# Optimization experiments

Hardware: AMD Instinct MI355X
Metric: run time of the kernel (lower is better)

## Reference

```python
import jax, jax.numpy as jnp
import numpy as np

N = 100000      # atoms
E = 1200000     # edges
N0 = 3125       # crystals
ORIG = 92
NBR = 41
AF = 64
NCONV = 3
HF = 128
EPS = 1e-5


def _bn(x, g, b):
    # training-mode BatchNorm1d: biased batch stats over axis 0
    m = jnp.mean(x, axis=0)
    v = jnp.var(x, axis=0)
    return (x - m) * jax.lax.rsqrt(v + EPS) * g + b


def setup_inputs() -> dict:
    key = jax.random.key(0)
    ks = jax.random.split(key, 16)
    inp = {}
    inp["atom_fea"] = jax.random.normal(ks[0], (N, ORIG), dtype=jnp.float32)
    inp["nbr_fea"] = jax.random.normal(ks[1], (E, NBR), dtype=jnp.float32)
    inp["self_fea_idx"] = jnp.sort(jax.random.randint(ks[2], (E,), 0, N))
    inp["nbr_fea_idx"] = jax.random.randint(ks[3], (E,), 0, N)
    inp["crystal_atom_idx"] = jnp.sort(jax.random.randint(ks[4], (N,), 0, N0))
    s = 0.05
    inp["emb_W"] = jax.random.normal(ks[5], (ORIG, AF), dtype=jnp.float32) * s
    inp["emb_b"] = jnp.zeros((AF,), dtype=jnp.float32)
    inp["conv_W"] = jax.random.normal(ks[6], (NCONV, 2 * AF + NBR, 2 * AF), dtype=jnp.float32) * s
    inp["conv_b"] = jnp.zeros((NCONV, 2 * AF), dtype=jnp.float32)
    inp["bn1_g"] = jnp.ones((NCONV, 2 * AF), dtype=jnp.float32)
    inp["bn1_b"] = jnp.zeros((NCONV, 2 * AF), dtype=jnp.float32)
    inp["bn2_g"] = jnp.ones((NCONV, AF), dtype=jnp.float32)
    inp["bn2_b"] = jnp.zeros((NCONV, AF), dtype=jnp.float32)
    inp["fc1_W"] = jax.random.normal(ks[7], (AF, HF), dtype=jnp.float32) * s
    inp["fc1_b"] = jnp.zeros((HF,), dtype=jnp.float32)
    inp["out_W"] = jax.random.normal(ks[8], (HF, 1), dtype=jnp.float32) * s
    inp["out_b"] = jnp.zeros((1,), dtype=jnp.float32)
    return inp


def reference(atom_fea, nbr_fea, self_fea_idx, nbr_fea_idx, crystal_atom_idx,
              emb_W, emb_b, conv_W, conv_b, bn1_g, bn1_b, bn2_g, bn2_b,
              fc1_W, fc1_b, out_W, out_b):
    sp = jax.nn.softplus
    x = atom_fea @ emb_W + emb_b                       # (N, AF)
    for i in range(NCONV):
        total = jnp.concatenate(
            [x[self_fea_idx], x[nbr_fea_idx], nbr_fea], axis=1)  # (E, 2*AF+NBR)
        total = total @ conv_W[i] + conv_b[i]                    # (E, 2*AF)
        total = _bn(total, bn1_g[i], bn1_b[i])
        filt, core = jnp.split(total, 2, axis=1)
        msg = jax.nn.sigmoid(filt) * sp(core)                    # (E, AF)
        summed = jax.ops.segment_sum(msg, self_fea_idx, num_segments=N)
        x = sp(x + _bn(summed, bn2_g[i], bn2_b[i]))
    # mean pooling over atoms per crystal
    crys_sum = jax.ops.segment_sum(x, crystal_atom_idx, num_segments=N0)
    counts = jax.ops.segment_sum(jnp.ones((N,), dtype=x.dtype),
                                 crystal_atom_idx, num_segments=N0)
    crys = crys_sum / jnp.maximum(counts, 1.0)[:, None]          # (N0, AF)
    crys = sp(sp(crys) @ fc1_W + fc1_b)                          # (N0, HF)
    return crys @ out_W + out_b                                  # (N0, 1)
```

## Files before the change

kernel.cpp:

```cpp
#include <hip/hip_runtime.h>
#include <hip/hip_bf16.h>
#include <hip/hip_fp16.h>

#define N_ATOM 100000
#define N_EDGE 1200000
#define N_CRYS 3125
#define EPSF 1e-5f

typedef __attribute__((ext_vector_type(8))) short bf16x8;
typedef __attribute__((ext_vector_type(4))) float f32x4;

__device__ __forceinline__ float fexp(float x) {
    return __builtin_amdgcn_exp2f(x * 1.4426950408889634f);
}
__device__ __forceinline__ float flog(float x) {
    return __builtin_amdgcn_logf(x) * 0.6931471805599453f;
}
__device__ __forceinline__ float frcp(float x) { return __builtin_amdgcn_rcpf(x); }

__device__ __forceinline__ float softplusf(float x) {
    return fmaxf(x, 0.f) + flog(1.f + fexp(-fabsf(x)));
}
__device__ __forceinline__ float sigmoidf(float x) {
    return frcp(1.f + fexp(-x));
}

__device__ __forceinline__ float ldf(const void* p, long i, int isf32) {
    return isf32 ? ((const float*)p)[i]
                 : __bfloat162float(((const __hip_bfloat16*)p)[i]);
}

__global__ void detect_dtype(const unsigned short* __restrict__ af,
                             int* __restrict__ flag) {
    __shared__ int cnt;
    if (threadIdx.x == 0) cnt = 0;
    __syncthreads();
    int c = 0;
    for (int i = threadIdx.x; i < 4096; i += 256) {
        int e = (af[i] >> 7) & 0xFF;
        if (e >= 100 && e <= 140) c++;
    }
    atomicAdd(&cnt, c);
    __syncthreads();
    if (threadIdx.x == 0) flag[0] = (cnt < 3300) ? 1 : 0;
}

__global__ void cvt_params(const void* embW, const void* embb, const void* bn1g,
                           const void* bn1b, const void* bn2g, const void* bn2b,
                           const void* fc1W, const void* fc1b, const void* outW,
                           const void* outb, const int* __restrict__ flag,
                           float* __restrict__ dst) {
    int f = flag[0];
    const void* ps[10] = {embW, embb, bn1g, bn1b, bn2g, bn2b, fc1W, fc1b, outW, outb};
    const int off[10]  = {0, 5888, 5952, 6336, 6720, 6912, 7104, 15296, 15424, 15552};
    const int n[10]    = {5888, 64, 384, 384, 192, 192, 8192, 128, 128, 1};
    for (int it = 0; it < 10; ++it)
        for (int i = threadIdx.x; i < n[it]; i += 256)
            dst[off[it] + i] = ldf(ps[it], i, f);
}


__global__ void pad_nbr(const void* __restrict__ nf, const int* __restrict__ flag,
                        __hip_bfloat16* __restrict__ np_) {
    int f = flag[0];
    long i = (long)blockIdx.x * 256 + threadIdx.x;
    long e = i >> 6;
    int  k = (int)(i & 63);
    float v = (k < 41) ? ldf(nf, e * 41 + k, f) : 0.f;
    np_[i] = __float2bfloat16(v);
}

__global__ void pack_W(const void* __restrict__ convW, const int* __restrict__ flag,
                       __hip_bfloat16* __restrict__ wf) {
    int f = flag[0];
    int b = blockIdx.x;
    int l = threadIdx.x;
    int t = b & 7;
    int c = (b >> 3) % 6;
    int layer = b / 48;
    int q = l >> 4, m = l & 15;
    for (int j = 0; j < 8; ++j) {
        int k = 32 * c + 8 * q + j;
        int n = 16 * t + m;
        float v = (k < 169) ? ldf(convW, ((long)layer * 169 + k) * 128 + n, f) : 0.f;
        wf[((((long)layer * 6 + c) * 8 + t) * 64 + l) * 8 + j] = __float2bfloat16(v);
    }
}

__global__ void embed(const void* __restrict__ af, const float* __restrict__ pb,
                      const int* __restrict__ flag,
                      float* __restrict__ x, __hip_bfloat16* __restrict__ xb) {
    __shared__ float A[4][92];
    int f = flag[0];
    int a0 = blockIdx.x * 4;
    for (int i = threadIdx.x; i < 4 * 92; i += 256)
        A[i / 92][i % 92] = ldf(af, (long)a0 * 92 + i, f);
    __syncthreads();
    int al = threadIdx.x >> 6, cc = threadIdx.x & 63;
    long ga = a0 + al;
    float s = pb[5888 + cc];
    for (int k = 0; k < 92; ++k)
        s += A[al][k] * pb[k * 64 + cc];
    x[ga * 64 + cc] = s;
    xb[ga * 64 + cc] = __float2bfloat16(s);
}

__global__ void build_rowptr(const int* __restrict__ idx, int len, int nseg,
                             int* __restrict__ rp) {
    int a = blockIdx.x * 256 + threadIdx.x;
    if (a > nseg) return;
    int lo = 0, hi = len;
    while (lo < hi) {
        int mid = (lo + hi) >> 1;
        if (idx[mid] < a) lo = mid + 1; else hi = mid;
    }
    rp[a] = lo;
}

__global__ __launch_bounds__(256) void conv_mm(
    const __hip_bfloat16* __restrict__ xb,
    const __hip_bfloat16* __restrict__ nbrp,
    const __hip_bfloat16* __restrict__ wf,
    const int* __restrict__ self_idx,
    const int* __restrict__ nbr_idx,
    __half* __restrict__ y16,
    float* __restrict__ part1) {
    __shared__ float lstat[256];
    int tid = threadIdx.x;
    lstat[tid] = 0.f;
    __syncthreads();

    int wv = tid >> 6;
    int l  = tid & 63;
    int q  = l >> 4;
    int m  = l & 15;
    long eb = (long)blockIdx.x * 64 + wv * 16;
    long e  = eb + m;
    long self_base = (long)self_idx[e] * 64;
    long nbr_base  = (long)nbr_idx[e]  * 64;
    long edge_base = e * 64;
    const short* xs = (const short*)xb;
    const short* ns = (const short*)nbrp;
    const bf16x8* wfp = (const bf16x8*)wf;

    f32x4 acc[8];
#pragma unroll
    for (int t = 0; t < 8; ++t) acc[t] = (f32x4){0.f, 0.f, 0.f, 0.f};

#pragma unroll
    for (int c = 0; c < 6; ++c) {
        const short* src;
        long off;
        if (c < 2)      { src = xs; off = self_base + 32 * c       + 8 * q; }
        else if (c < 4) { src = xs; off = nbr_base  + 32 * (c - 2) + 8 * q; }
        else            { src = ns; off = edge_base + 32 * (c - 4) + 8 * q; }
        bf16x8 a = *(const bf16x8*)(src + off);
#pragma unroll
        for (int t = 0; t < 8; ++t) {
            bf16x8 b = wfp[(c * 8 + t) * 64 + l];
            acc[t] = __builtin_amdgcn_mfma_f32_16x16x32_bf16(a, b, acc[t], 0, 0, 0);
        }
    }

#pragma unroll
    for (int t = 0; t < 8; ++t) {
        float s = 0.f, sq = 0.f;
#pragma unroll
        for (int r = 0; r < 4; ++r) {
            float v = acc[t][r];
            long er = eb + q * 4 + r;
            y16[er * 128 + 16 * t + m] = __float2half(v);
            s += v; sq += v * v;
        }
        s  += __shfl_xor(s, 16, 64);  s  += __shfl_xor(s, 32, 64);
        sq += __shfl_xor(sq, 16, 64); sq += __shfl_xor(sq, 32, 64);
        if (q == 0) {
            atomicAdd(&lstat[16 * t + m], s);
            atomicAdd(&lstat[128 + 16 * t + m], sq);
        }
    }
    __syncthreads();
    part1[(long)blockIdx.x * 256 + tid] = lstat[tid];
}

__global__ void reduce_rows(const float* __restrict__ src, float* __restrict__ dst,
                            int nrows, int rpb) {
    int ncols = blockDim.x;
    int col = threadIdx.x;
    long r0 = (long)blockIdx.x * rpb;
    long r1 = r0 + rpb; if (r1 > nrows) r1 = nrows;
    float s = 0.f;
    for (long r = r0; r < r1; ++r) s += src[r * ncols + col];
    dst[(long)blockIdx.x * ncols + col] = s;
}

__global__ __launch_bounds__(256) void conv_msg(
    const __half* __restrict__ y16,
    const int* __restrict__ rp,
    const float* __restrict__ stats1,
    const float* __restrict__ g1,
    const float* __restrict__ b1,
    float* __restrict__ summed,
    float* __restrict__ part2,
    float invE) {
    __shared__ float lp[128];
    int tid = threadIdx.x;
    if (tid < 128) lp[tid] = 0.f;
    __syncthreads();
    int wv = tid >> 6, j = tid & 63;
    int a = blockIdx.x * 4 + wv;
    if (a < N_ATOM) {
        float mf = stats1[j] * invE;
        float vf = stats1[128 + j] * invE - mf * mf;
        float mc = stats1[64 + j] * invE;
        float vc = stats1[192 + j] * invE - mc * mc;
        float rf = rsqrtf(fmaxf(vf, 0.f) + EPSF) * g1[j];
        float rc = rsqrtf(fmaxf(vc, 0.f) + EPSF) * g1[64 + j];
        float bf = b1[j];
        float bc = b1[64 + j];
        int e0 = rp[a], e1 = rp[a + 1];
        float s = 0.f;
        for (int e = e0; e < e1; ++e) {
            float fv = __half2float(y16[(long)e * 128 + j]);
            float cv = __half2float(y16[(long)e * 128 + 64 + j]);
            fv = (fv - mf) * rf + bf;
            cv = (cv - mc) * rc + bc;
            s += sigmoidf(fv) * softplusf(cv);
        }
        summed[(long)a * 64 + j] = s;
        atomicAdd(&lp[j], s);
        atomicAdd(&lp[64 + j], s * s);
    }
    __syncthreads();
    if (tid < 128) part2[(long)blockIdx.x * 128 + tid] = lp[tid];
}

__global__ void update_x(float* __restrict__ x, __hip_bfloat16* __restrict__ xb,
                         const float* __restrict__ summed,
                         const float* __restrict__ stats2,
                         const float* __restrict__ g2,
                         const float* __restrict__ b2,
                         float invN) {
    long i = (long)blockIdx.x * 256 + threadIdx.x;
    int j = (int)(i & 63);
    float m = stats2[j] * invN;
    float v = stats2[64 + j] * invN - m * m;
    float val = (summed[i] - m) * rsqrtf(fmaxf(v, 0.f) + EPSF) * g2[j] + b2[j];
    float sp = softplusf(x[i] + val);
    x[i] = sp;
    xb[i] = __float2bfloat16(sp);
}

__global__ void pool(const float* __restrict__ x, const int* __restrict__ cp,
                     float* __restrict__ crys_sp) {
    int wv = threadIdx.x >> 6, j = threadIdx.x & 63;
    int c = blockIdx.x * 4 + wv;
    if (c >= N_CRYS) return;
    int a0 = cp[c], a1 = cp[c + 1];
    float s = 0.f;
    for (int a = a0; a < a1; ++a) s += x[(long)a * 64 + j];
    float cnt = (float)(a1 - a0);
    float mean = s / fmaxf(cnt, 1.f);
    crys_sp[c * 64 + j] = softplusf(mean);
}

__global__ void head(const float* __restrict__ crys_sp,
                     const float* __restrict__ pb,
                     const int* __restrict__ flag,
                     void* __restrict__ out) {
    __shared__ float row[64];
    __shared__ float hred[128];
    int c = blockIdx.x, t = threadIdx.x;
    if (t < 64) row[t] = crys_sp[c * 64 + t];
    __syncthreads();
    float d = pb[15296 + t];
    for (int k = 0; k < 64; ++k)
        d += row[k] * pb[7104 + k * 128 + t];
    float h = softplusf(d);
    hred[t] = h * pb[15424 + t];
    __syncthreads();
    for (int off = 64; off > 0; off >>= 1) {
        if (t < off) hred[t] += hred[t + off];
        __syncthreads();
    }
    if (t == 0) {
        float v = hred[0] + pb[15552];
        if (flag[0]) ((float*)out)[c] = v;
        else         ((__hip_bfloat16*)out)[c] = __float2bfloat16(v);
    }
}

extern "C" void kernel_launch(void* const* d_in, const int* in_sizes, int n_in,
                              void* d_out, int out_size, void* d_ws, size_t ws_size,
                              hipStream_t stream) {
    const void* atom_fea = d_in[0];
    const void* nbr_fea  = d_in[1];
    const int* self_idx = (const int*)d_in[2];
    const int* nbr_idx  = (const int*)d_in[3];
    const int* crys_idx = (const int*)d_in[4];
    const void* emb_W  = d_in[5];
    const void* emb_b  = d_in[6];
    const void* conv_W = d_in[7];
    const void* bn1_g  = d_in[9];
    const void* bn1_b  = d_in[10];
    const void* bn2_g  = d_in[11];
    const void* bn2_b  = d_in[12];
    const void* fc1_W  = d_in[13];
    const void* fc1_b  = d_in[14];
    const void* out_W  = d_in[15];
    const void* out_b  = d_in[16];

    char* ws = (char*)d_ws;
    size_t off = 0;
    auto alloc = [&](size_t b) {
        void* p = ws + off;
        off = (off + b + 255) & ~(size_t)255;
        return p;
    };
    float*          x      = (float*)alloc((size_t)N_ATOM * 64 * 4);
    __hip_bfloat16* xb     = (__hip_bfloat16*)alloc((size_t)N_ATOM * 64 * 2);
    __hip_bfloat16* nbrp   = (__hip_bfloat16*)alloc((size_t)N_EDGE * 64 * 2);
    __hip_bfloat16* wfr    = (__hip_bfloat16*)alloc((size_t)3 * 24576 * 2);
    __half*         y16    = (__half*)alloc((size_t)N_EDGE * 128 * 2);
    float*          part1  = (float*)alloc((size_t)18750 * 256 * 4);
    float*          red1   = (float*)alloc((size_t)147 * 256 * 4);
    float*          stats1 = (float*)alloc(256 * 4);
    float*          summed = (float*)alloc((size_t)N_ATOM * 64 * 4);
    float*          part2  = (float*)alloc((size_t)25000 * 128 * 4);
    float*          red2   = (float*)alloc((size_t)98 * 128 * 4);
    float*          stats2 = (float*)alloc(128 * 4);
    int*            rp     = (int*)alloc((N_ATOM + 1) * 4);
    int*            cp     = (int*)alloc((N_CRYS + 1) * 4);
    float*          crysp  = (float*)alloc((size_t)N_CRYS * 64 * 4);
    float*          pbuf   = (float*)alloc(15553 * 4);
    int*            dflag  = (int*)alloc(4);
    (void)ws_size; (void)in_sizes; (void)n_in; (void)out_size;

    detect_dtype<<<1, 256, 0, stream>>>((const unsigned short*)atom_fea, dflag);
    cvt_params<<<1, 256, 0, stream>>>(emb_W, emb_b, bn1_g, bn1_b, bn2_g, bn2_b,
                                      fc1_W, fc1_b, out_W, out_b, dflag, pbuf);
    pad_nbr<<<N_EDGE * 64 / 256, 256, 0, stream>>>(nbr_fea, dflag, nbrp);
    pack_W<<<144, 64, 0, stream>>>(conv_W, dflag, wfr);
    embed<<<N_ATOM / 4, 256, 0, stream>>>(atom_fea, pbuf, dflag, x, xb);
    build_rowptr<<<(N_ATOM + 1 + 255) / 256, 256, 0, stream>>>(self_idx, N_EDGE, N_ATOM, rp);
    build_rowptr<<<(N_CRYS + 1 + 255) / 256, 256, 0, stream>>>(crys_idx, N_ATOM, N_CRYS, cp);

    for (int l = 0; l < 3; ++l) {
        conv_mm<<<N_EDGE / 64, 256, 0, stream>>>(xb, nbrp, wfr + (size_t)l * 24576,
                                                 self_idx, nbr_idx, y16, part1);
        reduce_rows<<<147, 256, 0, stream>>>(part1, red1, 18750, 128);
        reduce_rows<<<1, 256, 0, stream>>>(red1, stats1, 147, 147);
        conv_msg<<<N_ATOM / 4, 256, 0, stream>>>(y16, rp, stats1,
                                                 pbuf + 5952 + (size_t)l * 128,
                                                 pbuf + 6336 + (size_t)l * 128,
                                                 summed, part2, 1.f / (float)N_EDGE);
        reduce_rows<<<98, 128, 0, stream>>>(part2, red2, 25000, 256);
        reduce_rows<<<1, 128, 0, stream>>>(red2, stats2, 98, 98);
        update_x<<<N_ATOM * 64 / 256, 256, 0, stream>>>(x, xb, summed, stats2,
                                                        pbuf + 6720 + (size_t)l * 64,
                                                        pbuf + 6912 + (size_t)l * 64,
                                                        1.f / (float)N_ATOM);
    }

    pool<<<(N_CRYS + 3) / 4, 256, 0, stream>>>(x, cp, crysp);
    head<<<N_CRYS, 128, 0, stream>>>(crysp, pbuf, dflag, (void*)d_out);
}
```

Baseline: 2.408 ms.

## Stage conv weights in LDS and process two edge tiles per wave

The conv GEMM kernel now copies the packed 48 KB bf16 weight matrix into shared memory once per block. Each wave computes two 16-edge tiles that share every weight fragment, so a block covers 128 edges instead of 64. Grid size, partial-stat buffers and the reduction launches are resized to match. This cuts repeated global weight loads and halves the number of per-block stat partials. The cost is 48 KB of LDS per block, double the accumulator registers, and a staging copy at the start of every block, all of which may limit occupancy.

```diff
diff --git a/kernel.cpp b/kernel.cpp
--- a/kernel.cpp
+++ b/kernel.cpp
@@ -117,7 +117,7 @@
     rp[a] = lo;
 }
 
-__global__ __launch_bounds__(256) void conv_mm(
+__global__ __launch_bounds__(256, 4) void conv_mm16(
     const __hip_bfloat16* __restrict__ xb,
     const __hip_bfloat16* __restrict__ nbrp,
     const __hip_bfloat16* __restrict__ wf,
@@ -125,8 +125,14 @@
     const int* __restrict__ nbr_idx,
     __half* __restrict__ y16,
     float* __restrict__ part1) {
+    __shared__ __align__(16) __hip_bfloat16 wlds[24576];
     __shared__ float lstat[256];
     int tid = threadIdx.x;
+    {
+        const float4* wsrc = (const float4*)wf;
+        float4* wdst = (float4*)wlds;
+        for (int i = tid; i < 3072; i += 256) wdst[i] = wsrc[i];
+    }
     lstat[tid] = 0.f;
     __syncthreads();
 
@@ -134,31 +140,42 @@
     int l  = tid & 63;
     int q  = l >> 4;
     int m  = l & 15;
-    long eb = (long)blockIdx.x * 64 + wv * 16;
-    long e  = eb + m;
-    long self_base = (long)self_idx[e] * 64;
-    long nbr_base  = (long)nbr_idx[e]  * 64;
-    long edge_base = e * 64;
+    long eb = (long)blockIdx.x * 128 + wv * 32;
+    long sbase[2], nbase[2], ebase[2];
+#pragma unroll
+    for (int et = 0; et < 2; ++et) {
+        long e = eb + 16 * et + m;
+        sbase[et] = (long)self_idx[e] * 64;
+        nbase[et] = (long)nbr_idx[e]  * 64;
+        ebase[et] = e * 64;
+    }
     const short* xs = (const short*)xb;
     const short* ns = (const short*)nbrp;
-    const bf16x8* wfp = (const bf16x8*)wf;
-
-    f32x4 acc[8];
-#pragma unroll
-    for (int t = 0; t < 8; ++t) acc[t] = (f32x4){0.f, 0.f, 0.f, 0.f};
+    const bf16x8* wl = (const bf16x8*)wlds;
+
+    f32x4 acc[2][8];
+#pragma unroll
+    for (int et = 0; et < 2; ++et)
+#pragma unroll
+        for (int t = 0; t < 8; ++t) acc[et][t] = (f32x4){0.f, 0.f, 0.f, 0.f};
 
 #pragma unroll
     for (int c = 0; c < 6; ++c) {
-        const short* src;
-        long off;
-        if (c < 2)      { src = xs; off = self_base + 32 * c       + 8 * q; }
-        else if (c < 4) { src = xs; off = nbr_base  + 32 * (c - 2) + 8 * q; }
-        else            { src = ns; off = edge_base + 32 * (c - 4) + 8 * q; }
-        bf16x8 a = *(const bf16x8*)(src + off);
+        bf16x8 a[2];
+#pragma unroll
+        for (int et = 0; et < 2; ++et) {
+            const short* src;
+            long off;
+            if (c < 2)      { src = xs; off = sbase[et] + 32 * c       + 8 * q; }
+            else if (c < 4) { src = xs; off = nbase[et] + 32 * (c - 2) + 8 * q; }
+            else            { src = ns; off = ebase[et] + 32 * (c - 4) + 8 * q; }
+            a[et] = *(const bf16x8*)(src + off);
+        }
 #pragma unroll
         for (int t = 0; t < 8; ++t) {
-            bf16x8 b = wfp[(c * 8 + t) * 64 + l];
-            acc[t] = __builtin_amdgcn_mfma_f32_16x16x32_bf16(a, b, acc[t], 0, 0, 0);
+            bf16x8 b = wl[(c * 8 + t) * 64 + l];
+            acc[0][t] = __builtin_amdgcn_mfma_f32_16x16x32_bf16(a[0], b, acc[0][t], 0, 0, 0);
+            acc[1][t] = __builtin_amdgcn_mfma_f32_16x16x32_bf16(a[1], b, acc[1][t], 0, 0, 0);
         }
     }
 
@@ -166,11 +183,14 @@
     for (int t = 0; t < 8; ++t) {
         float s = 0.f, sq = 0.f;
 #pragma unroll
-        for (int r = 0; r < 4; ++r) {
-            float v = acc[t][r];
-            long er = eb + q * 4 + r;
-            y16[er * 128 + 16 * t + m] = __float2half(v);
-            s += v; sq += v * v;
+        for (int et = 0; et < 2; ++et) {
+#pragma unroll
+            for (int r = 0; r < 4; ++r) {
+                float v = acc[et][t][r];
+                long er = eb + 16 * et + q * 4 + r;
+                y16[er * 128 + 16 * t + m] = __float2half(v);
+                s += v; sq += v * v;
+            }
         }
         s  += __shfl_xor(s, 16, 64);  s  += __shfl_xor(s, 32, 64);
         sq += __shfl_xor(sq, 16, 64); sq += __shfl_xor(sq, 32, 64);
@@ -322,8 +342,8 @@
     __hip_bfloat16* nbrp   = (__hip_bfloat16*)alloc((size_t)N_EDGE * 64 * 2);
     __hip_bfloat16* wfr    = (__hip_bfloat16*)alloc((size_t)3 * 24576 * 2);
     __half*         y16    = (__half*)alloc((size_t)N_EDGE * 128 * 2);
-    float*          part1  = (float*)alloc((size_t)18750 * 256 * 4);
-    float*          red1   = (float*)alloc((size_t)147 * 256 * 4);
+    float*          part1  = (float*)alloc((size_t)9375 * 256 * 4);
+    float*          red1   = (float*)alloc((size_t)74 * 256 * 4);
     float*          stats1 = (float*)alloc(256 * 4);
     float*          summed = (float*)alloc((size_t)N_ATOM * 64 * 4);
     float*          part2  = (float*)alloc((size_t)25000 * 128 * 4);
@@ -339,17 +359,17 @@
     detect_dtype<<<1, 256, 0, stream>>>((const unsigned short*)atom_fea, dflag);
     cvt_params<<<1, 256, 0, stream>>>(emb_W, emb_b, bn1_g, bn1_b, bn2_g, bn2_b,
                                       fc1_W, fc1_b, out_W, out_b, dflag, pbuf);
-    pad_nbr<<<N_EDGE * 64 / 256, 256, 0, stream>>>(nbr_fea, dflag, nbrp);
+    pad_nbr<<<(int)((size_t)N_EDGE * 64 / 256), 256, 0, stream>>>(nbr_fea, dflag, nbrp);
     pack_W<<<144, 64, 0, stream>>>(conv_W, dflag, wfr);
     embed<<<N_ATOM / 4, 256, 0, stream>>>(atom_fea, pbuf, dflag, x, xb);
     build_rowptr<<<(N_ATOM + 1 + 255) / 256, 256, 0, stream>>>(self_idx, N_EDGE, N_ATOM, rp);
     build_rowptr<<<(N_CRYS + 1 + 255) / 256, 256, 0, stream>>>(crys_idx, N_ATOM, N_CRYS, cp);
 
     for (int l = 0; l < 3; ++l) {
-        conv_mm<<<N_EDGE / 64, 256, 0, stream>>>(xb, nbrp, wfr + (size_t)l * 24576,
-                                                 self_idx, nbr_idx, y16, part1);
-        reduce_rows<<<147, 256, 0, stream>>>(part1, red1, 18750, 128);
-        reduce_rows<<<1, 256, 0, stream>>>(red1, stats1, 147, 147);
+        conv_mm16<<<9375, 256, 0, stream>>>(xb, nbrp, wfr + (size_t)l * 24576,
+                                            self_idx, nbr_idx, y16, part1);
+        reduce_rows<<<74, 256, 0, stream>>>(part1, red1, 9375, 127);
+        reduce_rows<<<1, 256, 0, stream>>>(red1, stats1, 74, 74);
         conv_msg<<<N_ATOM / 4, 256, 0, stream>>>(y16, rp, stats1,
                                                  pbuf + 5952 + (size_t)l * 128,
                                                  pbuf + 6336 + (size_t)l * 128,
```

Result: faster. 2.154 ms (-10.5%).
